# Kernel optimization log

Hardware: AMD Instinct MI355X
Metric: run time of the kernel (lower is better)

Reference implementation:

```python
import jax, jax.numpy as jnp
import numpy as np

T, H, I, E, S = 1024, 1024, 512, 64, 2  # tokens, hidden, intermediate, routed experts, shared experts
G, TOPK_GROUP, K = 8, 4, 8              # n_group, topk_group, num_experts_per_tok


def setup_inputs() -> dict:
    key = jax.random.key(0)
    ks = jax.random.split(key, 6)
    scale = 0.02
    x = jax.random.normal(ks[0], (T, H), dtype=jnp.float32)
    gate_w = jax.random.normal(ks[1], (E, H), dtype=jnp.float32) * scale   # MoEGate.weight [E,H]
    w_gu = jax.random.normal(ks[2], (E, H, 2 * I), dtype=jnp.float32) * scale  # gate_up_proj.weight.T per expert
    w_d = jax.random.normal(ks[3], (E, I, H), dtype=jnp.float32) * scale       # down_proj.weight.T per expert
    s_gu = jax.random.normal(ks[4], (S, H, 2 * I), dtype=jnp.float32) * scale  # shared experts
    s_d = jax.random.normal(ks[5], (S, I, H), dtype=jnp.float32) * scale
    return {"x": x, "gate_w": gate_w, "w_gu": w_gu, "w_d": w_d, "s_gu": s_gu, "s_d": s_d}


def _moe_forward(x, gate_w, w_gu, w_d, s_gu, s_d):
    t, h = x.shape
    e = w_gu.shape[0]
    i = w_gu.shape[2] // 2
    group_size = e // G

    # ---- shared experts (always active), summed ----
    sh = jnp.einsum('th,shf->stf', x, s_gu)            # [S,T,2I]
    shared = jnp.einsum('stf,sfh->th', jax.nn.silu(sh[..., :i]) * sh[..., i:], s_d)

    # ---- grouped top-k gating ----
    logits = x @ gate_w.T                               # [T,E]
    group_logits = logits.reshape(t, G, group_size)
    gw, gi = jax.lax.top_k(group_logits, TOPK_GROUP)    # [T,G,topk_group]
    gw = gw.reshape(t, G * TOPK_GROUP)
    gi = gi.reshape(t, G * TOPK_GROUP)
    topk_w, ti = jax.lax.top_k(gw, K)                   # [T,K]
    sel_group = ti // TOPK_GROUP
    expert_in_group = jnp.take_along_axis(gi, ti, axis=1)
    topk_idx = sel_group * group_size + expert_in_group # [T,K]
    topk_w = topk_w / (topk_w.sum(axis=-1, keepdims=True) + 1e-20)  # norm_topk_prob

    # ---- combine weights: sparse [T,E] scatter of top-k weights ----
    combine = jnp.zeros((t, e), x.dtype).at[jnp.arange(t)[:, None], topk_idx].add(topk_w)

    # ---- routed experts: dense grouped GEMM, zero-weighted where unselected ----
    gu = jnp.einsum('th,ehf->etf', x, w_gu)             # [E,T,2I]
    hidden = jax.nn.silu(gu[..., :i]) * gu[..., i:]     # [E,T,I]
    y = jnp.einsum('eti,eih->eth', hidden, w_d)         # [E,T,H]
    routed = jnp.einsum('eth,te->th', y, combine)

    return shared + routed


def reference(x, gate_w, w_gu, w_d, s_gu, s_d):
    return _moe_forward(x, gate_w, w_gu, w_d, s_gu, s_d)
```

## Files before the change

### kernel.cpp

```cpp
#include <hip/hip_runtime.h>
#include <hip/hip_bf16.h>

#define T_ 1024
#define H_ 1024
#define I_ 512
#define E_ 64
#define S_ 2
#define NJOB 66
#define KSEL 8
#define GRP 8
#define GSIZE 8
#define TKG 4
#define ROWS_TOTAL (T_*KSEL + S_*T_)
#define SH0 (T_*KSEL)
#define SH1 (T_*KSEL + T_)

typedef __attribute__((ext_vector_type(8))) __bf16 bf16x8;
typedef __attribute__((ext_vector_type(8))) unsigned short u16x8;
typedef __attribute__((ext_vector_type(4))) unsigned short u16x4;
typedef __attribute__((ext_vector_type(4))) float f32x4;

__device__ inline unsigned short f2bf(float f) {
    unsigned u = __float_as_uint(f);
    u += 0x7FFFu + ((u >> 16) & 1u);
    return (unsigned short)(u >> 16);
}

__device__ inline unsigned pk2bf(float a, float b) {
    unsigned short ua = __builtin_bit_cast(unsigned short, (__bf16)a);
    unsigned short ub = __builtin_bit_cast(unsigned short, (__bf16)b);
    return (unsigned)ua | ((unsigned)ub << 16);
}

__device__ inline void async16(const void* g, void* l) {
    __builtin_amdgcn_global_load_lds(
        (const __attribute__((address_space(1))) unsigned int*)g,
        (__attribute__((address_space(3))) unsigned int*)(uintptr_t)l,
        16, 0, 0);
}

__global__ __launch_bounds__(256) void cvt_x_kernel(const float* __restrict__ x,
                                                    unsigned short* __restrict__ xb) {
    int i = (blockIdx.x * 256 + threadIdx.x) * 4;
    f32x4 v = *(const f32x4*)(x + i);
    u16x4 o;
    o[0] = f2bf(v[0]); o[1] = f2bf(v[1]); o[2] = f2bf(v[2]); o[3] = f2bf(v[3]);
    *(u16x4*)(xb + i) = o;
}

__global__ __launch_bounds__(256) void gate_kernel(const float* __restrict__ x,
                                                   const float* __restrict__ gate_w,
                                                   int* __restrict__ counts,
                                                   int* __restrict__ topk_idx,
                                                   float* __restrict__ topk_w) {
    __shared__ float Wt[64 * 65];
    __shared__ float Xs[4 * 65];
    __shared__ float lg[4 * 65];

    int tid = threadIdx.x;
    int t0 = blockIdx.x * 4;
    int e = tid & 63;
    int wq = tid >> 6;
    int er = tid >> 2;
    int kq = (tid & 3) * 16;
    int xk = tid & 63;

    float acc = 0.f;
    for (int kc = 0; kc < 16; ++kc) {
        const float* wp = gate_w + er * H_ + kc * 64 + kq;
        f32x4 w0 = *(const f32x4*)(wp);
        f32x4 w1 = *(const f32x4*)(wp + 4);
        f32x4 w2 = *(const f32x4*)(wp + 8);
        f32x4 w3 = *(const f32x4*)(wp + 12);
        float xv = x[(size_t)(t0 + wq) * H_ + kc * 64 + xk];
        __syncthreads();
#pragma unroll
        for (int i = 0; i < 4; ++i) {
            Wt[(kq + i) * 65 + er] = w0[i];
            Wt[(kq + 4 + i) * 65 + er] = w1[i];
            Wt[(kq + 8 + i) * 65 + er] = w2[i];
            Wt[(kq + 12 + i) * 65 + er] = w3[i];
        }
        Xs[wq * 65 + xk] = xv;
        __syncthreads();
#pragma unroll 8
        for (int k = 0; k < 64; ++k)
            acc += Wt[k * 65 + e] * Xs[wq * 65 + k];
    }
    lg[wq * 65 + e] = acc;
    __syncthreads();

    if (tid < 4) {
        int t = t0 + tid;
        const float* L = &lg[tid * 65];
        float cv[GRP * TKG];
        int   ce[GRP * TKG];
        for (int g = 0; g < GRP; ++g) {
            unsigned used = 0;
            for (int r = 0; r < TKG; ++r) {
                float best = -INFINITY; int bi = 0;
                for (int j = 0; j < GSIZE; ++j) {
                    if (used & (1u << j)) continue;
                    float v = L[g * GSIZE + j];
                    if (v > best) { best = v; bi = j; }
                }
                used |= 1u << bi;
                cv[g * TKG + r] = best;
                ce[g * TKG + r] = g * GSIZE + bi;
            }
        }
        float sv[KSEL]; int si[KSEL];
        unsigned used = 0;
        float sum = 0.0f;
        for (int r = 0; r < KSEL; ++r) {
            float best = -INFINITY; int bi = 0;
            for (int j = 0; j < GRP * TKG; ++j) {
                if (used & (1u << j)) continue;
                if (cv[j] > best) { best = cv[j]; bi = j; }
            }
            used |= 1u << bi;
            sv[r] = best; si[r] = ce[bi];
            sum += best;
        }
        float inv = 1.0f / (sum + 1e-20f);
        for (int r = 0; r < KSEL; ++r) {
            topk_idx[t * KSEL + r] = si[r];
            topk_w[t * KSEL + r] = sv[r] * inv;
            atomicAdd(&counts[si[r]], 1);
        }
    }
}

__global__ __launch_bounds__(128) void prefix_kernel(const int* __restrict__ counts,
                                                     int* __restrict__ offsets,
                                                     int* __restrict__ cursor) {
    __shared__ int c[NJOB];
    int tid = threadIdx.x;
    int own = 0;
    if (tid < NJOB) {
        own = (tid < E_) ? counts[tid] : T_;
        c[tid] = own;
    }
    __syncthreads();
    for (int d = 1; d < NJOB; d <<= 1) {
        int v = 0;
        if (tid < NJOB && tid >= d) v = c[tid - d];
        __syncthreads();
        if (tid < NJOB) c[tid] += v;
        __syncthreads();
    }
    if (tid < NJOB) {
        int excl = c[tid] - own;
        offsets[tid] = excl;
        cursor[tid] = excl;
    }
    if (tid == 0) offsets[NJOB] = ROWS_TOTAL;
}

__global__ __launch_bounds__(256) void place_kernel(const int* __restrict__ topk_idx,
                                                    const int* __restrict__ offsets,
                                                    int* __restrict__ cursor,
                                                    int* __restrict__ row_token,
                                                    int* __restrict__ slot_map) {
    int p = blockIdx.x * 256 + threadIdx.x;
    if (p < T_ * KSEL) {
        int t = p >> 3;
        int e = topk_idx[p];
        int slot = atomicAdd(&cursor[e], 1);
        row_token[slot] = t;
        slot_map[p] = slot;
    } else if (p < T_ * KSEL + S_ * T_) {
        int q = p - T_ * KSEL;
        int s = q >> 10;
        int t = q & (T_ - 1);
        int slot = offsets[E_ + s] + t;
        row_token[slot] = t;
    }
}

__global__ __launch_bounds__(512) void gateup_kernel(const unsigned short* __restrict__ xb,
                                                     const float* __restrict__ w_gu,
                                                     const float* __restrict__ s_gu,
                                                     const int* __restrict__ offsets,
                                                     const int* __restrict__ row_token,
                                                     unsigned short* __restrict__ hidden) {
    int job = blockIdx.x, mt = blockIdx.y, nt = blockIdx.z;
    int seg = offsets[job];
    int cnt = offsets[job + 1] - seg;
    int m0 = mt * 256;
    if (m0 >= cnt) return;
    const float* W = (job < E_) ? (w_gu + (size_t)job * H_ * (2 * I_))
                                : (s_gu + (size_t)(job - E_) * H_ * (2 * I_));
    int n0 = nt * 64;

    __shared__ unsigned short As[256 * 64];
    __shared__ unsigned short Bg[64 * 64];
    __shared__ unsigned short Bu[64 * 64];

    int tid = threadIdx.x;
    int wv = tid >> 6, lane = tid & 63, lrow = lane & 15, lq = lane >> 4;

    const unsigned short* asrc[4];
#pragma unroll
    for (int i = 0; i < 4; ++i) {
        int d = i * 512 + tid;
        int row = d >> 3;
        int kc = (d & 7) ^ (row & 7);
        int r = m0 + row;
        int gi = seg + (r < cnt ? r : 0);
        asrc[i] = xb + (size_t)row_token[gi] * H_ + kc * 8;
    }

    int bk = (tid & 31) * 2;
    int bn = (tid >> 5) * 4;
    int c0 = bk >> 3;
    int hb = (bk & 7) * 2;
    const float* bbase = W + (size_t)bk * (2 * I_) + n0 + bn;

    f32x4 accg[2][4], accu[2][4];
    f32x4 zero = {0.f, 0.f, 0.f, 0.f};
#pragma unroll
    for (int a = 0; a < 2; ++a)
#pragma unroll
        for (int c = 0; c < 4; ++c) { accg[a][c] = zero; accu[a][c] = zero; }

    f32x4 g[2], u[2];
#pragma unroll
    for (int r = 0; r < 2; ++r) {
        g[r] = *(const f32x4*)(bbase + (size_t)r * (2 * I_));
        u[r] = *(const f32x4*)(bbase + (size_t)r * (2 * I_) + I_);
    }

    for (int kt = 0; kt < H_ / 64; ++kt) {
        int ko = kt * 64;
#pragma unroll
        for (int i = 0; i < 4; ++i)
            async16(asrc[i] + ko, &As[(i * 512 + tid) * 8]);

#pragma unroll
        for (int j = 0; j < 4; ++j) {
            int nj = bn + j;
            int byteoff = nj * 128 + ((c0 ^ (nj & 7)) * 16) + hb;
            *(unsigned*)((char*)Bg + byteoff) = pk2bf(g[0][j], g[1][j]);
            *(unsigned*)((char*)Bu + byteoff) = pk2bf(u[0][j], u[1][j]);
        }

        {
            int kn = ((kt + 1) & 15) * 64;
            const float* bp = bbase + (size_t)kn * (2 * I_);
#pragma unroll
            for (int r = 0; r < 2; ++r) {
                g[r] = *(const f32x4*)(bp + (size_t)r * (2 * I_));
                u[r] = *(const f32x4*)(bp + (size_t)r * (2 * I_) + I_);
            }
        }
        __syncthreads();

#pragma unroll
        for (int kk = 0; kk < 2; ++kk) {
            bf16x8 a[2];
#pragma unroll
            for (int rb = 0; rb < 2; ++rb) {
                int R = wv * 32 + rb * 16 + lrow;
                a[rb] = *(const bf16x8*)&As[R * 64 + (((lq + kk * 4) ^ (R & 7)) * 8)];
            }
#pragma unroll
            for (int cb = 0; cb < 4; ++cb) {
                int n = cb * 16 + lrow;
                int koff = ((lq + kk * 4) ^ (n & 7)) * 8;
                bf16x8 bg = *(const bf16x8*)&Bg[n * 64 + koff];
                bf16x8 bu = *(const bf16x8*)&Bu[n * 64 + koff];
#pragma unroll
                for (int rb = 0; rb < 2; ++rb) {
                    accg[rb][cb] = __builtin_amdgcn_mfma_f32_16x16x32_bf16(a[rb], bg, accg[rb][cb], 0, 0, 0);
                    accu[rb][cb] = __builtin_amdgcn_mfma_f32_16x16x32_bf16(a[rb], bu, accu[rb][cb], 0, 0, 0);
                }
            }
        }
        __syncthreads();
    }

#pragma unroll
    for (int rb = 0; rb < 2; ++rb)
#pragma unroll
        for (int cb = 0; cb < 4; ++cb)
#pragma unroll
            for (int r = 0; r < 4; ++r) {
                int row = wv * 32 + rb * 16 + lq * 4 + r;
                if (m0 + row < cnt) {
                    float gg = accg[rb][cb][r];
                    float uu = accu[rb][cb][r];
                    float hh = gg / (1.0f + __expf(-gg)) * uu;
                    hidden[(size_t)(seg + m0 + row) * I_ + n0 + cb * 16 + lrow] = f2bf(hh);
                }
            }
}

__global__ __launch_bounds__(512) void down_kernel(const unsigned short* __restrict__ hidden,
                                                   const float* __restrict__ w_d,
                                                   const float* __restrict__ s_d,
                                                   const int* __restrict__ offsets,
                                                   float* __restrict__ yrow) {
    int job = blockIdx.x, mt = blockIdx.y, nt = blockIdx.z;
    int seg = offsets[job];
    int cnt = offsets[job + 1] - seg;
    int m0 = mt * 256;
    if (m0 >= cnt) return;
    const float* W = (job < E_) ? (w_d + (size_t)job * I_ * H_)
                                : (s_d + (size_t)(job - E_) * I_ * H_);
    int n0 = nt * 64;

    __shared__ unsigned short As[256 * 64];
    __shared__ unsigned short Bs[64 * 64];

    int tid = threadIdx.x;
    int wv = tid >> 6, lane = tid & 63, lrow = lane & 15, lq = lane >> 4;

    const unsigned short* asrc[4];
#pragma unroll
    for (int i = 0; i < 4; ++i) {
        int d = i * 512 + tid;
        int row = d >> 3;
        int kc = (d & 7) ^ (row & 7);
        int r = m0 + row;
        int gi = seg + (r < cnt ? r : 0);
        asrc[i] = hidden + (size_t)gi * I_ + kc * 8;
    }

    int bk = (tid & 31) * 2;
    int bn = (tid >> 5) * 4;
    int c0 = bk >> 3;
    int hb = (bk & 7) * 2;
    const float* bbase = W + (size_t)bk * H_ + n0 + bn;

    f32x4 acc[2][4];
    f32x4 zero = {0.f, 0.f, 0.f, 0.f};
#pragma unroll
    for (int a = 0; a < 2; ++a)
#pragma unroll
        for (int c = 0; c < 4; ++c) acc[a][c] = zero;

    f32x4 d4[2];
#pragma unroll
    for (int r = 0; r < 2; ++r)
        d4[r] = *(const f32x4*)(bbase + (size_t)r * H_);

    for (int kt = 0; kt < I_ / 64; ++kt) {
        int ko = kt * 64;
#pragma unroll
        for (int i = 0; i < 4; ++i)
            async16(asrc[i] + ko, &As[(i * 512 + tid) * 8]);

#pragma unroll
        for (int j = 0; j < 4; ++j) {
            int nj = bn + j;
            int byteoff = nj * 128 + ((c0 ^ (nj & 7)) * 16) + hb;
            *(unsigned*)((char*)Bs + byteoff) = pk2bf(d4[0][j], d4[1][j]);
        }
        {
            int kn = ((kt + 1) & 7) * 64;
            const float* bp = bbase + (size_t)kn * H_;
#pragma unroll
            for (int r = 0; r < 2; ++r)
                d4[r] = *(const f32x4*)(bp + (size_t)r * H_);
        }
        __syncthreads();

#pragma unroll
        for (int kk = 0; kk < 2; ++kk) {
            bf16x8 a[2];
#pragma unroll
            for (int rb = 0; rb < 2; ++rb) {
                int R = wv * 32 + rb * 16 + lrow;
                a[rb] = *(const bf16x8*)&As[R * 64 + (((lq + kk * 4) ^ (R & 7)) * 8)];
            }
#pragma unroll
            for (int cb = 0; cb < 4; ++cb) {
                int n = cb * 16 + lrow;
                bf16x8 b = *(const bf16x8*)&Bs[n * 64 + (((lq + kk * 4) ^ (n & 7)) * 8)];
#pragma unroll
                for (int rb = 0; rb < 2; ++rb)
                    acc[rb][cb] = __builtin_amdgcn_mfma_f32_16x16x32_bf16(a[rb], b, acc[rb][cb], 0, 0, 0);
            }
        }
        __syncthreads();
    }

#pragma unroll
    for (int rb = 0; rb < 2; ++rb)
#pragma unroll
        for (int r = 0; r < 4; ++r) {
            int row = wv * 32 + rb * 16 + lq * 4 + r;
            if (m0 + row < cnt) {
#pragma unroll
                for (int cb = 0; cb < 4; ++cb)
                    yrow[(size_t)(seg + m0 + row) * H_ + n0 + cb * 16 + lrow] = acc[rb][cb][r];
            }
        }
}

__global__ __launch_bounds__(256) void reduce_kernel(const float* __restrict__ yrow,
                                                     const int* __restrict__ slot_map,
                                                     const float* __restrict__ topk_w,
                                                     float* __restrict__ out) {
    int t = blockIdx.x;
    __shared__ int sl[KSEL];
    __shared__ float sw[KSEL];
    if (threadIdx.x < KSEL) {
        sl[threadIdx.x] = slot_map[t * KSEL + threadIdx.x];
        sw[threadIdx.x] = topk_w[t * KSEL + threadIdx.x];
    }
    __syncthreads();
    int col = threadIdx.x * 4;
    f32x4 a0 = *(const f32x4*)(yrow + (size_t)(SH0 + t) * H_ + col);
    f32x4 a1 = *(const f32x4*)(yrow + (size_t)(SH1 + t) * H_ + col);
    f32x4 acc;
#pragma unroll
    for (int j = 0; j < 4; ++j) acc[j] = a0[j] + a1[j];
#pragma unroll
    for (int k = 0; k < KSEL; ++k) {
        f32x4 v = *(const f32x4*)(yrow + (size_t)sl[k] * H_ + col);
        float w = sw[k];
#pragma unroll
        for (int j = 0; j < 4; ++j) acc[j] += v[j] * w;
    }
    *(f32x4*)(out + (size_t)t * H_ + col) = acc;
}

extern "C" void kernel_launch(void* const* d_in, const int* in_sizes, int n_in,
                              void* d_out, int out_size, void* d_ws, size_t ws_size,
                              hipStream_t stream) {
    const float* x      = (const float*)d_in[0];
    const float* gate_w = (const float*)d_in[1];
    const float* w_gu   = (const float*)d_in[2];
    const float* w_d    = (const float*)d_in[3];
    const float* s_gu   = (const float*)d_in[4];
    const float* s_d    = (const float*)d_in[5];
    float* out = (float*)d_out;

    char* ws = (char*)d_ws;
    size_t off = 0;
    auto carve = [&](size_t bytes) -> void* {
        void* p = ws + off;
        off += (bytes + 255) & ~(size_t)255;
        return p;
    };
    int* counts            = (int*)carve(NJOB * 4);
    int* offsets           = (int*)carve((NJOB + 1) * 4);
    int* cursor            = (int*)carve(NJOB * 4);
    int* topk_idx          = (int*)carve(T_ * KSEL * 4);
    float* topk_w          = (float*)carve(T_ * KSEL * 4);
    int* row_token         = (int*)carve(ROWS_TOTAL * 4);
    int* slot_map          = (int*)carve(T_ * KSEL * 4);
    unsigned short* xb     = (unsigned short*)carve((size_t)T_ * H_ * 2);
    unsigned short* hidden = (unsigned short*)carve((size_t)ROWS_TOTAL * I_ * 2);
    float* yrow            = (float*)carve((size_t)ROWS_TOTAL * H_ * 4);

    hipMemsetAsync(counts, 0, NJOB * 4, stream);

    cvt_x_kernel<<<(T_ * H_ / 4) / 256, 256, 0, stream>>>(x, xb);
    gate_kernel<<<T_ / 4, 256, 0, stream>>>(x, gate_w, counts, topk_idx, topk_w);
    prefix_kernel<<<1, 128, 0, stream>>>(counts, offsets, cursor);
    place_kernel<<<(ROWS_TOTAL + 255) / 256, 256, 0, stream>>>(topk_idx, offsets,
                                                               cursor, row_token, slot_map);
    gateup_kernel<<<dim3(NJOB, T_ / 256, I_ / 64), 512, 0, stream>>>(xb, w_gu, s_gu, offsets,
                                                                     row_token, hidden);
    down_kernel<<<dim3(NJOB, T_ / 256, H_ / 64), 512, 0, stream>>>(hidden, w_d, s_d, offsets,
                                                                   yrow);
    reduce_kernel<<<T_, 256, 0, stream>>>(yrow, slot_map, topk_w, out);
}
```

Baseline: 621.7 us.

## Double-buffer LDS tiles, shrink M tile to 128, reorder grid and skip idle waves

Both grouped GEMM kernels now use 256-thread blocks with 128-row M tiles and double-buffered LDS for the A and B tiles. The next A async copy and B global load are issued after a single barrier and overlap the current tile's MFMAs, which removes one __syncthreads per k-step. The grid is reordered so N tiles vary fastest, and waves whose rows are all beyond the expert's count skip their MFMAs. Smaller tiles cut padding waste for experts with few rows, at the cost of loading each weight tile more often and more per-thread B registers.

```diff
diff --git a/kernel.cpp b/kernel.cpp
--- a/kernel.cpp
+++ b/kernel.cpp
@@ -178,32 +178,33 @@
     }
 }
 
-__global__ __launch_bounds__(512) void gateup_kernel(const unsigned short* __restrict__ xb,
+__global__ __launch_bounds__(256) void gateup_kernel(const unsigned short* __restrict__ xb,
                                                      const float* __restrict__ w_gu,
                                                      const float* __restrict__ s_gu,
                                                      const int* __restrict__ offsets,
                                                      const int* __restrict__ row_token,
                                                      unsigned short* __restrict__ hidden) {
-    int job = blockIdx.x, mt = blockIdx.y, nt = blockIdx.z;
+    int nt = blockIdx.x, mt = blockIdx.y, job = blockIdx.z;
     int seg = offsets[job];
     int cnt = offsets[job + 1] - seg;
-    int m0 = mt * 256;
+    int m0 = mt * 128;
     if (m0 >= cnt) return;
     const float* W = (job < E_) ? (w_gu + (size_t)job * H_ * (2 * I_))
                                 : (s_gu + (size_t)(job - E_) * H_ * (2 * I_));
     int n0 = nt * 64;
 
-    __shared__ unsigned short As[256 * 64];
-    __shared__ unsigned short Bg[64 * 64];
-    __shared__ unsigned short Bu[64 * 64];
+    __shared__ unsigned short As[2][128 * 64];
+    __shared__ unsigned short Bg[2][64 * 64];
+    __shared__ unsigned short Bu[2][64 * 64];
 
     int tid = threadIdx.x;
     int wv = tid >> 6, lane = tid & 63, lrow = lane & 15, lq = lane >> 4;
+    bool active = (m0 + wv * 32) < cnt;
 
     const unsigned short* asrc[4];
 #pragma unroll
     for (int i = 0; i < 4; ++i) {
-        int d = i * 512 + tid;
+        int d = i * 256 + tid;
         int row = d >> 3;
         int kc = (d & 7) ^ (row & 7);
         int r = m0 + row;
@@ -211,10 +212,10 @@
         asrc[i] = xb + (size_t)row_token[gi] * H_ + kc * 8;
     }
 
-    int bk = (tid & 31) * 2;
-    int bn = (tid >> 5) * 4;
+    int bk = (tid & 15) * 4;
+    int bn = (tid >> 4) * 4;
     int c0 = bk >> 3;
-    int hb = (bk & 7) * 2;
+    int h8 = (bk & 4) * 2;
     const float* bbase = W + (size_t)bk * (2 * I_) + n0 + bn;
 
     f32x4 accg[2][4], accu[2][4];
@@ -224,60 +225,66 @@
 #pragma unroll
         for (int c = 0; c < 4; ++c) { accg[a][c] = zero; accu[a][c] = zero; }
 
-    f32x4 g[2], u[2];
-#pragma unroll
-    for (int r = 0; r < 2; ++r) {
+    f32x4 g[4], u[4];
+#pragma unroll
+    for (int r = 0; r < 4; ++r) {
         g[r] = *(const f32x4*)(bbase + (size_t)r * (2 * I_));
         u[r] = *(const f32x4*)(bbase + (size_t)r * (2 * I_) + I_);
     }
-
-    for (int kt = 0; kt < H_ / 64; ++kt) {
-        int ko = kt * 64;
-#pragma unroll
-        for (int i = 0; i < 4; ++i)
-            async16(asrc[i] + ko, &As[(i * 512 + tid) * 8]);
-
+#pragma unroll
+    for (int i = 0; i < 4; ++i)
+        async16(asrc[i], &As[0][(i * 256 + tid) * 8]);
+
+    for (int kt = 0; kt < 16; ++kt) {
+        int c = kt & 1;
 #pragma unroll
         for (int j = 0; j < 4; ++j) {
             int nj = bn + j;
-            int byteoff = nj * 128 + ((c0 ^ (nj & 7)) * 16) + hb;
-            *(unsigned*)((char*)Bg + byteoff) = pk2bf(g[0][j], g[1][j]);
-            *(unsigned*)((char*)Bu + byteoff) = pk2bf(u[0][j], u[1][j]);
-        }
-
-        {
-            int kn = ((kt + 1) & 15) * 64;
-            const float* bp = bbase + (size_t)kn * (2 * I_);
-#pragma unroll
-            for (int r = 0; r < 2; ++r) {
+            int byteoff = nj * 128 + ((c0 ^ (nj & 7)) * 16) + h8;
+            uint2 vg, vu;
+            vg.x = pk2bf(g[0][j], g[1][j]); vg.y = pk2bf(g[2][j], g[3][j]);
+            vu.x = pk2bf(u[0][j], u[1][j]); vu.y = pk2bf(u[2][j], u[3][j]);
+            *(uint2*)((char*)Bg[c] + byteoff) = vg;
+            *(uint2*)((char*)Bu[c] + byteoff) = vu;
+        }
+        __syncthreads();
+
+        if (kt < 15) {
+            int ko = (kt + 1) * 64;
+#pragma unroll
+            for (int i = 0; i < 4; ++i)
+                async16(asrc[i] + ko, &As[c ^ 1][(i * 256 + tid) * 8]);
+            const float* bp = bbase + (size_t)ko * (2 * I_);
+#pragma unroll
+            for (int r = 0; r < 4; ++r) {
                 g[r] = *(const f32x4*)(bp + (size_t)r * (2 * I_));
                 u[r] = *(const f32x4*)(bp + (size_t)r * (2 * I_) + I_);
             }
         }
-        __syncthreads();
-
-#pragma unroll
-        for (int kk = 0; kk < 2; ++kk) {
-            bf16x8 a[2];
-#pragma unroll
-            for (int rb = 0; rb < 2; ++rb) {
-                int R = wv * 32 + rb * 16 + lrow;
-                a[rb] = *(const bf16x8*)&As[R * 64 + (((lq + kk * 4) ^ (R & 7)) * 8)];
-            }
-#pragma unroll
-            for (int cb = 0; cb < 4; ++cb) {
-                int n = cb * 16 + lrow;
-                int koff = ((lq + kk * 4) ^ (n & 7)) * 8;
-                bf16x8 bg = *(const bf16x8*)&Bg[n * 64 + koff];
-                bf16x8 bu = *(const bf16x8*)&Bu[n * 64 + koff];
+
+        if (active) {
+#pragma unroll
+            for (int kk = 0; kk < 2; ++kk) {
+                bf16x8 a[2];
 #pragma unroll
                 for (int rb = 0; rb < 2; ++rb) {
-                    accg[rb][cb] = __builtin_amdgcn_mfma_f32_16x16x32_bf16(a[rb], bg, accg[rb][cb], 0, 0, 0);
-                    accu[rb][cb] = __builtin_amdgcn_mfma_f32_16x16x32_bf16(a[rb], bu, accu[rb][cb], 0, 0, 0);
-                }
-            }
-        }
-        __syncthreads();
+                    int R = wv * 32 + rb * 16 + lrow;
+                    a[rb] = *(const bf16x8*)&As[c][R * 64 + (((lq + kk * 4) ^ (R & 7)) * 8)];
+                }
+#pragma unroll
+                for (int cb = 0; cb < 4; ++cb) {
+                    int n = cb * 16 + lrow;
+                    int koff = ((lq + kk * 4) ^ (n & 7)) * 8;
+                    bf16x8 bg = *(const bf16x8*)&Bg[c][n * 64 + koff];
+                    bf16x8 bu = *(const bf16x8*)&Bu[c][n * 64 + koff];
+#pragma unroll
+                    for (int rb = 0; rb < 2; ++rb) {
+                        accg[rb][cb] = __builtin_amdgcn_mfma_f32_16x16x32_bf16(a[rb], bg, accg[rb][cb], 0, 0, 0);
+                        accu[rb][cb] = __builtin_amdgcn_mfma_f32_16x16x32_bf16(a[rb], bu, accu[rb][cb], 0, 0, 0);
+                    }
+                }
+            }
+        }
     }
 
 #pragma unroll
@@ -296,30 +303,31 @@
             }
 }
 
-__global__ __launch_bounds__(512) void down_kernel(const unsigned short* __restrict__ hidden,
+__global__ __launch_bounds__(256) void down_kernel(const unsigned short* __restrict__ hidden,
                                                    const float* __restrict__ w_d,
                                                    const float* __restrict__ s_d,
                                                    const int* __restrict__ offsets,
                                                    float* __restrict__ yrow) {
-    int job = blockIdx.x, mt = blockIdx.y, nt = blockIdx.z;
+    int nt = blockIdx.x, mt = blockIdx.y, job = blockIdx.z;
     int seg = offsets[job];
     int cnt = offsets[job + 1] - seg;
-    int m0 = mt * 256;
+    int m0 = mt * 128;
     if (m0 >= cnt) return;
     const float* W = (job < E_) ? (w_d + (size_t)job * I_ * H_)
                                 : (s_d + (size_t)(job - E_) * I_ * H_);
     int n0 = nt * 64;
 
-    __shared__ unsigned short As[256 * 64];
-    __shared__ unsigned short Bs[64 * 64];
+    __shared__ unsigned short As[2][128 * 64];
+    __shared__ unsigned short Bs[2][64 * 64];
 
     int tid = threadIdx.x;
     int wv = tid >> 6, lane = tid & 63, lrow = lane & 15, lq = lane >> 4;
+    bool active = (m0 + wv * 32) < cnt;
 
     const unsigned short* asrc[4];
 #pragma unroll
     for (int i = 0; i < 4; ++i) {
-        int d = i * 512 + tid;
+        int d = i * 256 + tid;
         int row = d >> 3;
         int kc = (d & 7) ^ (row & 7);
         int r = m0 + row;
@@ -327,10 +335,10 @@
         asrc[i] = hidden + (size_t)gi * I_ + kc * 8;
     }
 
-    int bk = (tid & 31) * 2;
-    int bn = (tid >> 5) * 4;
+    int bk = (tid & 15) * 4;
+    int bn = (tid >> 4) * 4;
     int c0 = bk >> 3;
-    int hb = (bk & 7) * 2;
+    int h8 = (bk & 4) * 2;
     const float* bbase = W + (size_t)bk * H_ + n0 + bn;
 
     f32x4 acc[2][4];
@@ -340,50 +348,56 @@
 #pragma unroll
         for (int c = 0; c < 4; ++c) acc[a][c] = zero;
 
-    f32x4 d4[2];
-#pragma unroll
-    for (int r = 0; r < 2; ++r)
+    f32x4 d4[4];
+#pragma unroll
+    for (int r = 0; r < 4; ++r)
         d4[r] = *(const f32x4*)(bbase + (size_t)r * H_);
-
-    for (int kt = 0; kt < I_ / 64; ++kt) {
-        int ko = kt * 64;
-#pragma unroll
-        for (int i = 0; i < 4; ++i)
-            async16(asrc[i] + ko, &As[(i * 512 + tid) * 8]);
-
+#pragma unroll
+    for (int i = 0; i < 4; ++i)
+        async16(asrc[i], &As[0][(i * 256 + tid) * 8]);
+
+    for (int kt = 0; kt < 8; ++kt) {
+        int c = kt & 1;
 #pragma unroll
         for (int j = 0; j < 4; ++j) {
             int nj = bn + j;
-            int byteoff = nj * 128 + ((c0 ^ (nj & 7)) * 16) + hb;
-            *(unsigned*)((char*)Bs + byteoff) = pk2bf(d4[0][j], d4[1][j]);
-        }
-        {
-            int kn = ((kt + 1) & 7) * 64;
-            const float* bp = bbase + (size_t)kn * H_;
-#pragma unroll
-            for (int r = 0; r < 2; ++r)
+            int byteoff = nj * 128 + ((c0 ^ (nj & 7)) * 16) + h8;
+            uint2 vb;
+            vb.x = pk2bf(d4[0][j], d4[1][j]); vb.y = pk2bf(d4[2][j], d4[3][j]);
+            *(uint2*)((char*)Bs[c] + byteoff) = vb;
+        }
+        __syncthreads();
+
+        if (kt < 7) {
+            int ko = (kt + 1) * 64;
+#pragma unroll
+            for (int i = 0; i < 4; ++i)
+                async16(asrc[i] + ko, &As[c ^ 1][(i * 256 + tid) * 8]);
+            const float* bp = bbase + (size_t)ko * H_;
+#pragma unroll
+            for (int r = 0; r < 4; ++r)
                 d4[r] = *(const f32x4*)(bp + (size_t)r * H_);
         }
-        __syncthreads();
-
-#pragma unroll
-        for (int kk = 0; kk < 2; ++kk) {
-            bf16x8 a[2];
-#pragma unroll
-            for (int rb = 0; rb < 2; ++rb) {
-                int R = wv * 32 + rb * 16 + lrow;
-                a[rb] = *(const bf16x8*)&As[R * 64 + (((lq + kk * 4) ^ (R & 7)) * 8)];
-            }
-#pragma unroll
-            for (int cb = 0; cb < 4; ++cb) {
-                int n = cb * 16 + lrow;
-                bf16x8 b = *(const bf16x8*)&Bs[n * 64 + (((lq + kk * 4) ^ (n & 7)) * 8)];
-#pragma unroll
-                for (int rb = 0; rb < 2; ++rb)
-                    acc[rb][cb] = __builtin_amdgcn_mfma_f32_16x16x32_bf16(a[rb], b, acc[rb][cb], 0, 0, 0);
-            }
-        }
-        __syncthreads();
+
+        if (active) {
+#pragma unroll
+            for (int kk = 0; kk < 2; ++kk) {
+                bf16x8 a[2];
+#pragma unroll
+                for (int rb = 0; rb < 2; ++rb) {
+                    int R = wv * 32 + rb * 16 + lrow;
+                    a[rb] = *(const bf16x8*)&As[c][R * 64 + (((lq + kk * 4) ^ (R & 7)) * 8)];
+                }
+#pragma unroll
+                for (int cb = 0; cb < 4; ++cb) {
+                    int n = cb * 16 + lrow;
+                    bf16x8 b = *(const bf16x8*)&Bs[c][n * 64 + (((lq + kk * 4) ^ (n & 7)) * 8)];
+#pragma unroll
+                    for (int rb = 0; rb < 2; ++rb)
+                        acc[rb][cb] = __builtin_amdgcn_mfma_f32_16x16x32_bf16(a[rb], b, acc[rb][cb], 0, 0, 0);
+                }
+            }
+        }
     }
 
 #pragma unroll
@@ -463,9 +477,9 @@
     prefix_kernel<<<1, 128, 0, stream>>>(counts, offsets, cursor);
     place_kernel<<<(ROWS_TOTAL + 255) / 256, 256, 0, stream>>>(topk_idx, offsets,
                                                                cursor, row_token, slot_map);
-    gateup_kernel<<<dim3(NJOB, T_ / 256, I_ / 64), 512, 0, stream>>>(xb, w_gu, s_gu, offsets,
+    gateup_kernel<<<dim3(I_ / 64, T_ / 128, NJOB), 256, 0, stream>>>(xb, w_gu, s_gu, offsets,
                                                                      row_token, hidden);
-    down_kernel<<<dim3(NJOB, T_ / 256, H_ / 64), 512, 0, stream>>>(hidden, w_d, s_d, offsets,
+    down_kernel<<<dim3(H_ / 64, T_ / 128, NJOB), 256, 0, stream>>>(hidden, w_d, s_d, offsets,
                                                                    yrow);
     reduce_kernel<<<T_, 256, 0, stream>>>(yrow, slot_map, topk_w, out);
 }
```

Result: slower. 717.7 us (+15.4%).
